# Kernel optimization log

Hardware: AMD Instinct MI355X
Metric: run time of the kernel (lower is better)

## Reference

```python
import jax, jax.numpy as jnp
import numpy as np

HIDDEN = 1024
NUM_HEADS = 8
HEAD_DIM = HIDDEN // NUM_HEADS
MAX_BACKWARD = 11   # context_left - 1
MAX_FORWARD = 12    # context_right
SPAN = MAX_BACKWARD + MAX_FORWARD + 1  # 24

B, U, W, C = 8, 16, 128, 151


def setup_inputs() -> dict:
    key = jax.random.key(0)
    kq, kk, kp = jax.random.split(key, 3)
    queries = jax.random.normal(kq, (B, U, W, NUM_HEADS, HEAD_DIM), dtype=jnp.float32)
    keys = jax.random.normal(kk, (B, U, C, NUM_HEADS, HEAD_DIM), dtype=jnp.float32)
    # glorot-ish scale for pos_proj (hidden, num_heads*head_dim)
    pos_proj = jax.random.normal(kp, (HIDDEN, NUM_HEADS * HEAD_DIM), dtype=jnp.float32) * (1.0 / np.sqrt(HIDDEN))
    return {"queries": queries, "keys": keys, "pos_proj": pos_proj}


def _sinusoid_emb(pos_proj):
    # positions: max_backward .. -max_forward (descending), shape (SPAN,)
    pos = jnp.arange(MAX_BACKWARD, -(MAX_FORWARD + 1), -1, dtype=jnp.float32)
    num_ts = HIDDEN // 2
    inv_ts = jnp.ones((num_ts,), dtype=jnp.float32)  # module uses ones
    scaled = pos[:, None] * inv_ts[None, :]          # (SPAN, HIDDEN/2)
    signal = jnp.concatenate([jnp.sin(scaled), jnp.cos(scaled)], axis=-1)  # (SPAN, HIDDEN)
    proj = signal @ pos_proj                         # (SPAN, N*H)
    return proj.reshape(SPAN, NUM_HEADS, HEAD_DIM)


def _relative_shift(term_bd, context_size):
    # term_bd: (B, N, U, W, SPAN) -> (B, N, U, W, C)
    b, n, u, w, _ = term_bd.shape
    pad = context_size + 1 - SPAN
    padded = jnp.pad(term_bd, ((0, 0), (0, 0), (0, 0), (0, 0), (0, pad)))
    flat = padded.reshape(b, n, u, w * (context_size + 1))
    sliced = flat[:, :, :, : w * context_size]
    return sliced.reshape(b, n, u, w, context_size)


def reference(queries, keys, pos_proj):
    context_size = keys.shape[2]
    sin_emb = _sinusoid_emb(pos_proj)                      # (SPAN, N, H)
    qp = jnp.transpose(queries, (0, 3, 1, 2, 4))           # (B, N, U, W, H)
    kp = jnp.transpose(keys, (0, 3, 1, 4, 2))              # (B, N, U, H, C)
    term_ac = jnp.matmul(qp, kp)                           # (B, N, U, W, C)
    # term_bd: query-position interaction, (B, N, U, W, SPAN)
    term_bd = jnp.einsum("bnuwh,fnh->bnuwf", qp, sin_emb)
    term_bd = _relative_shift(term_bd, context_size)       # (B, N, U, W, C)
    return term_ac + term_bd
```

## Files before the change

kernel.cpp:

```cpp
#include <hip/hip_runtime.h>
#include <cmath>

#define NHEADS 8
#define HDIM 128
#define SPAN 24
#define U_ 16
#define W_ 128
#define C_ 151
#define HID 1024

typedef unsigned short ushort8v __attribute__((ext_vector_type(8)));
typedef __bf16 bf16x8 __attribute__((ext_vector_type(8)));
typedef float f32x4 __attribute__((ext_vector_type(4)));

__device__ inline unsigned short f2bf(float f) {
    union { float f; unsigned u; } v; v.f = f;
    unsigned r = v.u + 0x7FFFu + ((v.u >> 16) & 1u);
    return (unsigned short)(r >> 16);
}
__device__ inline float bf2f(unsigned short u) {
    union { unsigned u; float f; } v; v.u = ((unsigned)u) << 16;
    return v.f;
}

__global__ void k_partial(const float* __restrict__ pp, float* __restrict__ part) {
    const int t = threadIdx.x;
    const int row0 = blockIdx.x * 16;
    float4 s = make_float4(0.f, 0.f, 0.f, 0.f);
    #pragma unroll
    for (int i = 0; i < 16; ++i) {
        float4 v = *(const float4*)(pp + (size_t)(row0 + i) * HID + t * 4);
        s.x += v.x; s.y += v.y; s.z += v.z; s.w += v.w;
    }
    *(float4*)(part + (size_t)blockIdx.x * HID + t * 4) = s;
}

struct SC { float s[SPAN]; float c[SPAN]; };

__global__ void k_emb(const float* __restrict__ part, unsigned short* __restrict__ emb, SC sc) {
    const int j = blockIdx.x * 256 + threadIdx.x;
    float s1 = 0.f, s2 = 0.f;
    #pragma unroll 4
    for (int i = 0; i < 32; ++i) s1 += part[(size_t)i * HID + j];
    #pragma unroll 4
    for (int i = 32; i < 64; ++i) s2 += part[(size_t)i * HID + j];
    #pragma unroll
    for (int f = 0; f < SPAN; ++f)
        emb[(size_t)f * HID + j] = f2bf(sc.s[f] * s1 + sc.c[f] * s2);
}

#define KEXT_BYTES (176 * 256)
#define BD_PITCH 25

__global__ __launch_bounds__(512, 6) void k_main(const float* __restrict__ q,
                                                 const float* __restrict__ k,
                                                 const unsigned short* __restrict__ emb,
                                                 float* __restrict__ out) {
    __shared__ __align__(16) char lds_raw[KEXT_BYTES + W_ * BD_PITCH * 2];
    unsigned short* bd = (unsigned short*)(lds_raw + KEXT_BYTES);

    const int bid = (blockIdx.x & 7) * 128 + (blockIdx.x >> 3);
    const int n = bid & 7;
    const int u = (bid >> 3) & 15;
    const int b = bid >> 7;

    const size_t qbase = ((size_t)(b * U_ + u) * W_) * HID + n * HDIM;
    const size_t kbase = ((size_t)(b * U_ + u) * C_) * HID + n * HDIM;
    const size_t obase = ((size_t)((b * NHEADS + n) * U_ + u)) * (W_ * C_);

    const int tid = threadIdx.x;
    const int lane = tid & 63;
    const int wave = tid >> 6;
    const int w0 = wave * 16;
    const int lr = lane & 15;
    const int lk = lane >> 4;

    for (int ui = tid; ui < 176 * 16; ui += 512) {
        const int r = ui >> 4, u16 = ui & 15;
        const int dst = r * 256 + ((u16 * 16) ^ ((r & 7) << 4));
        ushort8v val;
        if (r < C_) {
            const float* src = k + kbase + (size_t)r * HID + u16 * 8;
            float4 f0 = *(const float4*)src;
            float4 f1 = *(const float4*)(src + 4);
            val[0] = f2bf(f0.x); val[1] = f2bf(f0.y); val[2] = f2bf(f0.z); val[3] = f2bf(f0.w);
            val[4] = f2bf(f1.x); val[5] = f2bf(f1.y); val[6] = f2bf(f1.z); val[7] = f2bf(f1.w);
        } else if (r < 175) {
            val = *(const ushort8v*)(emb + (size_t)(r - C_) * HID + n * HDIM + u16 * 8);
        } else {
            val = (ushort8v)(unsigned short)0;
        }
        *(ushort8v*)(lds_raw + dst) = val;
    }

    const float* qrow = q + qbase + (size_t)(w0 + lr) * HID + lk * 8;
    float4 qa[8];
    #pragma unroll
    for (int kk = 0; kk < 4; ++kk) {
        qa[2 * kk]     = *(const float4*)(qrow + kk * 32);
        qa[2 * kk + 1] = *(const float4*)(qrow + kk * 32 + 4);
    }
    bf16x8 qf[4];
    #pragma unroll
    for (int kk = 0; kk < 4; ++kk) {
        float4 a0 = qa[2 * kk];
        float4 a1 = qa[2 * kk + 1];
        ushort8v au;
        au[0] = f2bf(a0.x); au[1] = f2bf(a0.y); au[2] = f2bf(a0.z); au[3] = f2bf(a0.w);
        au[4] = f2bf(a1.x); au[5] = f2bf(a1.y); au[6] = f2bf(a1.z); au[7] = f2bf(a1.w);
        qf[kk] = __builtin_bit_cast(bf16x8, au);
    }
    __syncthreads();

    f32x4 acc[11];
    #pragma unroll
    for (int j = 0; j < 11; ++j) acc[j] = (f32x4)(0.f);

    #pragma unroll
    for (int kk = 0; kk < 4; ++kk) {
        #pragma unroll
        for (int j = 0; j < 11; ++j) {
            const int r = j * 16 + lr;
            const int byt = r * 256 + (((kk * 64) + (lk * 16)) ^ ((r & 7) << 4));
            bf16x8 bf = __builtin_bit_cast(bf16x8, *(const ushort8v*)(lds_raw + byt));
            acc[j] = __builtin_amdgcn_mfma_f32_16x16x32_bf16(qf[kk], bf, acc[j], 0, 0, 0);
        }
    }

    {
        const int c9 = 144 + lr;
        if (c9 >= C_) {
            const int f = c9 - C_;
            #pragma unroll
            for (int reg = 0; reg < 4; ++reg) {
                const int w = w0 + lk * 4 + reg;
                bd[w * BD_PITCH + f] = f2bf(acc[9][reg]);
            }
        }
        const int f10 = 9 + lr;
        if (f10 < SPAN) {
            #pragma unroll
            for (int reg = 0; reg < 4; ++reg) {
                const int w = w0 + lk * 4 + reg;
                bd[w * BD_PITCH + f10] = f2bf(acc[10][reg]);
            }
        }
    }

    #pragma unroll
    for (int j = 0; j < 10; ++j) {
        const int c = j * 16 + lr;
        if (c < C_) {
            #pragma unroll
            for (int reg = 0; reg < 4; ++reg) {
                const int w = w0 + lk * 4 + reg;
                float v = acc[j][reg];
                const int d = c - w;
                if (d >= 0 && d < SPAN) v += bf2f(bd[w * BD_PITCH + d]);
                out[obase + (size_t)w * C_ + c] = v;
            }
        }
    }
}

extern "C" void kernel_launch(void* const* d_in, const int* in_sizes, int n_in,
                              void* d_out, int out_size, void* d_ws, size_t ws_size,
                              hipStream_t stream) {
    const float* queries = (const float*)d_in[0];
    const float* keys    = (const float*)d_in[1];
    const float* posproj = (const float*)d_in[2];
    float* out = (float*)d_out;

    float* part = (float*)d_ws;
    unsigned short* emb = (unsigned short*)((char*)d_ws + 64 * HID * 4);

    SC sc;
    for (int f = 0; f < SPAN; ++f) {
        float p = (float)(11 - f);
        sc.s[f] = sinf(p);
        sc.c[f] = cosf(p);
    }

    k_partial<<<64, 256, 0, stream>>>(posproj, part);
    k_emb<<<4, 256, 0, stream>>>(part, emb, sc);
    k_main<<<1024, 512, 0, stream>>>(queries, keys, emb, out);
}
```

Before: 59.23 us.

## Make main kernel process four tiles per block with double-buffered LDS prefetch

Result: faster. 57.94 us (-2.2%).

```diff
diff --git a/kernel.cpp b/kernel.cpp
--- a/kernel.cpp
+++ b/kernel.cpp
@@ -21,6 +21,12 @@
 __device__ inline float bf2f(unsigned short u) {
     union { unsigned u; float f; } v; v.u = ((unsigned)u) << 16;
     return v.f;
+}
+__device__ inline ushort8v cvt8(float4 a, float4 b) {
+    ushort8v v;
+    v[0] = f2bf(a.x); v[1] = f2bf(a.y); v[2] = f2bf(a.z); v[3] = f2bf(a.w);
+    v[4] = f2bf(b.x); v[5] = f2bf(b.y); v[6] = f2bf(b.z); v[7] = f2bf(b.w);
+    return v;
 }
 
 __global__ void k_partial(const float* __restrict__ pp, float* __restrict__ part) {
@@ -37,7 +43,7 @@
 
 struct SC { float s[SPAN]; float c[SPAN]; };
 
-__global__ void k_emb(const float* __restrict__ part, unsigned short* __restrict__ emb, SC sc) {
+__global__ void k_emb(const float* __restrict__ part, float* __restrict__ emb, SC sc) {
     const int j = blockIdx.x * 256 + threadIdx.x;
     float s1 = 0.f, s2 = 0.f;
     #pragma unroll 4
@@ -46,27 +52,79 @@
     for (int i = 32; i < 64; ++i) s2 += part[(size_t)i * HID + j];
     #pragma unroll
     for (int f = 0; f < SPAN; ++f)
-        emb[(size_t)f * HID + j] = f2bf(sc.s[f] * s1 + sc.c[f] * s2);
-}
-
-#define KEXT_BYTES (176 * 256)
+        emb[(size_t)f * HID + j] = sc.s[f] * s1 + sc.c[f] * s2;
+}
+
+#define KB 45056
 #define BD_PITCH 25
-
-__global__ __launch_bounds__(512, 6) void k_main(const float* __restrict__ q,
+#define NITER 4
+
+
+#define STAGE_LOAD(TILE)                                                        \
+    {                                                                           \
+        const int n_ = (TILE) & 7;                                              \
+        const int u_ = ((TILE) >> 3) & 15;                                      \
+        const int b_ = (TILE) >> 7;                                             \
+        const size_t kb_ = ((size_t)(b_ * U_ + u_) * C_) * HID + n_ * HDIM;     \
+        _Pragma("unroll")                                                       \
+        for (int it = 0; it < 4; ++it) {                                        \
+            const int ui = it * 512 + tid;                                      \
+            const int r = ui >> 4, u16 = ui & 15;                               \
+            const float* src = k + kb_ + (size_t)r * HID + u16 * 8;             \
+            pf0[it] = *(const float4*)src;                                      \
+            pf1[it] = *(const float4*)(src + 4);                                \
+        }                                                                       \
+        {                                                                       \
+            const int ui = 4 * 512 + tid;                                       \
+            const int r = ui >> 4, u16 = ui & 15;                               \
+            const float* src = (r < C_)                                         \
+                ? (k + kb_ + (size_t)r * HID + u16 * 8)                         \
+                : (embf + (size_t)(r - C_) * HID + n_ * HDIM + u16 * 8);        \
+            pf0[4] = *(const float4*)src;                                       \
+            pf1[4] = *(const float4*)(src + 4);                                 \
+        }                                                                       \
+        if (tid < 256) {                                                        \
+            const int r = 160 + (tid >> 4), u16 = tid & 15;                     \
+            if (r < 175) {                                                      \
+                const float* src = embf + (size_t)(r - C_) * HID + n_ * HDIM + u16 * 8; \
+                pt0 = *(const float4*)src;                                      \
+                pt1 = *(const float4*)(src + 4);                                \
+            }                                                                   \
+        }                                                                       \
+        const size_t qb_ = ((size_t)(b_ * U_ + u_) * W_) * HID + n_ * HDIM;     \
+        const float* qrow_ = q + qb_ + (size_t)(w0 + lr) * HID + lk * 8;        \
+        _Pragma("unroll")                                                       \
+        for (int kk = 0; kk < 4; ++kk) {                                        \
+            qpf[2 * kk]     = *(const float4*)(qrow_ + kk * 32);                \
+            qpf[2 * kk + 1] = *(const float4*)(qrow_ + kk * 32 + 4);            \
+        }                                                                       \
+    }
+
+#define STAGE_WRITE(BUF)                                                        \
+    {                                                                           \
+        _Pragma("unroll")                                                       \
+        for (int it = 0; it < 5; ++it) {                                        \
+            const int ui = it * 512 + tid;                                      \
+            const int r = ui >> 4, u16 = ui & 15;                               \
+            const int dst = r * 256 + ((u16 * 16) ^ ((r & 7) << 4));            \
+            *(ushort8v*)((BUF) + dst) = cvt8(pf0[it], pf1[it]);                 \
+        }                                                                       \
+        if (tid < 256) {                                                        \
+            const int r = 160 + (tid >> 4), u16 = tid & 15;                     \
+            const int dst = r * 256 + ((u16 * 16) ^ ((r & 7) << 4));            \
+            ushort8v v_;                                                        \
+            if (r < 175) v_ = cvt8(pt0, pt1);                                   \
+            else         v_ = (ushort8v)(unsigned short)0;                      \
+            *(ushort8v*)((BUF) + dst) = v_;                                     \
+        }                                                                       \
+    }
+
+__global__ __launch_bounds__(512, 2) void k_main(const float* __restrict__ q,
                                                  const float* __restrict__ k,
-                                                 const unsigned short* __restrict__ emb,
+                                                 const float* __restrict__ embf,
                                                  float* __restrict__ out) {
-    __shared__ __align__(16) char lds_raw[KEXT_BYTES + W_ * BD_PITCH * 2];
-    unsigned short* bd = (unsigned short*)(lds_raw + KEXT_BYTES);
-
-    const int bid = (blockIdx.x & 7) * 128 + (blockIdx.x >> 3);
-    const int n = bid & 7;
-    const int u = (bid >> 3) & 15;
-    const int b = bid >> 7;
-
-    const size_t qbase = ((size_t)(b * U_ + u) * W_) * HID + n * HDIM;
-    const size_t kbase = ((size_t)(b * U_ + u) * C_) * HID + n * HDIM;
-    const size_t obase = ((size_t)((b * NHEADS + n) * U_ + u)) * (W_ * C_);
+    __shared__ __align__(16) char lds_raw[2 * KB + W_ * BD_PITCH * 2];
+    unsigned short* bd = (unsigned short*)(lds_raw + 2 * KB);
 
     const int tid = threadIdx.x;
     const int lane = tid & 63;
@@ -75,91 +133,86 @@
     const int lr = lane & 15;
     const int lk = lane >> 4;
 
-    for (int ui = tid; ui < 176 * 16; ui += 512) {
-        const int r = ui >> 4, u16 = ui & 15;
-        const int dst = r * 256 + ((u16 * 16) ^ ((r & 7) << 4));
-        ushort8v val;
-        if (r < C_) {
-            const float* src = k + kbase + (size_t)r * HID + u16 * 8;
-            float4 f0 = *(const float4*)src;
-            float4 f1 = *(const float4*)(src + 4);
-            val[0] = f2bf(f0.x); val[1] = f2bf(f0.y); val[2] = f2bf(f0.z); val[3] = f2bf(f0.w);
-            val[4] = f2bf(f1.x); val[5] = f2bf(f1.y); val[6] = f2bf(f1.z); val[7] = f2bf(f1.w);
-        } else if (r < 175) {
-            val = *(const ushort8v*)(emb + (size_t)(r - C_) * HID + n * HDIM + u16 * 8);
-        } else {
-            val = (ushort8v)(unsigned short)0;
+    const int logical = (blockIdx.x & 7) * 32 + (blockIdx.x >> 3);
+    const int tile0 = logical * NITER;
+
+    float4 pf0[5], pf1[5], pt0, pt1, qpf[8];
+
+    STAGE_LOAD(tile0);
+    STAGE_WRITE(lds_raw);
+    __syncthreads();
+
+    for (int i = 0; i < NITER; ++i) {
+        const int tile = tile0 + i;
+        char* bufc = lds_raw + (i & 1) * KB;
+        char* bufn = lds_raw + ((i & 1) ^ 1) * KB;
+
+        bf16x8 qf[4];
+        #pragma unroll
+        for (int kk = 0; kk < 4; ++kk)
+            qf[kk] = __builtin_bit_cast(bf16x8, cvt8(qpf[2 * kk], qpf[2 * kk + 1]));
+
+        if (i + 1 < NITER) STAGE_LOAD(tile + 1);
+
+        f32x4 acc[11];
+        #pragma unroll
+        for (int j = 0; j < 11; ++j) acc[j] = (f32x4)(0.f);
+
+        #pragma unroll
+        for (int kk = 0; kk < 4; ++kk) {
+            #pragma unroll
+            for (int j = 0; j < 11; ++j) {
+                const int r = j * 16 + lr;
+                const int byt = r * 256 + (((kk * 64) + (lk * 16)) ^ ((r & 7) << 4));
+                bf16x8 bf = __builtin_bit_cast(bf16x8, *(const ushort8v*)(bufc + byt));
+                acc[j] = __builtin_amdgcn_mfma_f32_16x16x32_bf16(qf[kk], bf, acc[j], 0, 0, 0);
+            }
         }
-        *(ushort8v*)(lds_raw + dst) = val;
-    }
-
-    const float* qrow = q + qbase + (size_t)(w0 + lr) * HID + lk * 8;
-    float4 qa[8];
-    #pragma unroll
-    for (int kk = 0; kk < 4; ++kk) {
-        qa[2 * kk]     = *(const float4*)(qrow + kk * 32);
-        qa[2 * kk + 1] = *(const float4*)(qrow + kk * 32 + 4);
-    }
-    bf16x8 qf[4];
-    #pragma unroll
-    for (int kk = 0; kk < 4; ++kk) {
-        float4 a0 = qa[2 * kk];
-        float4 a1 = qa[2 * kk + 1];
-        ushort8v au;
-        au[0] = f2bf(a0.x); au[1] = f2bf(a0.y); au[2] = f2bf(a0.z); au[3] = f2bf(a0.w);
-        au[4] = f2bf(a1.x); au[5] = f2bf(a1.y); au[6] = f2bf(a1.z); au[7] = f2bf(a1.w);
-        qf[kk] = __builtin_bit_cast(bf16x8, au);
-    }
-    __syncthreads();
-
-    f32x4 acc[11];
-    #pragma unroll
-    for (int j = 0; j < 11; ++j) acc[j] = (f32x4)(0.f);
-
-    #pragma unroll
-    for (int kk = 0; kk < 4; ++kk) {
-        #pragma unroll
-        for (int j = 0; j < 11; ++j) {
-            const int r = j * 16 + lr;
-            const int byt = r * 256 + (((kk * 64) + (lk * 16)) ^ ((r & 7) << 4));
-            bf16x8 bf = __builtin_bit_cast(bf16x8, *(const ushort8v*)(lds_raw + byt));
-            acc[j] = __builtin_amdgcn_mfma_f32_16x16x32_bf16(qf[kk], bf, acc[j], 0, 0, 0);
+
+        if (i + 1 < NITER) STAGE_WRITE(bufn);
+
+        {
+            const int c9 = 144 + lr;
+            if (c9 >= C_) {
+                const int f = c9 - C_;
+                #pragma unroll
+                for (int reg = 0; reg < 4; ++reg) {
+                    const int w = w0 + lk * 4 + reg;
+                    bd[w * BD_PITCH + f] = f2bf(acc[9][reg]);
+                }
+            }
+            const int f10 = 9 + lr;
+            if (f10 < SPAN) {
+                #pragma unroll
+                for (int reg = 0; reg < 4; ++reg) {
+                    const int w = w0 + lk * 4 + reg;
+                    bd[w * BD_PITCH + f10] = f2bf(acc[10][reg]);
+                }
+            }
         }
-    }
-
-    {
-        const int c9 = 144 + lr;
-        if (c9 >= C_) {
-            const int f = c9 - C_;
+
+        {
+            const int n_ = tile & 7;
+            const int u_ = (tile >> 3) & 15;
+            const int b_ = tile >> 7;
+            const size_t ob_ = ((size_t)((b_ * NHEADS + n_) * U_ + u_)) * (W_ * C_);
             #pragma unroll
-            for (int reg = 0; reg < 4; ++reg) {
-                const int w = w0 + lk * 4 + reg;
-                bd[w * BD_PITCH + f] = f2bf(acc[9][reg]);
+            for (int j = 0; j < 10; ++j) {
+                const int c = j * 16 + lr;
+                if (c < C_) {
+                    #pragma unroll
+                    for (int reg = 0; reg < 4; ++reg) {
+                        const int w = w0 + lk * 4 + reg;
+                        float v = acc[j][reg];
+                        const int d = c - w;
+                        if (d >= 0 && d < SPAN) v += bf2f(bd[w * BD_PITCH + d]);
+                        out[ob_ + (size_t)w * C_ + c] = v;
+                    }
+                }
             }
         }
-        const int f10 = 9 + lr;
-        if (f10 < SPAN) {
-            #pragma unroll
-            for (int reg = 0; reg < 4; ++reg) {
-                const int w = w0 + lk * 4 + reg;
-                bd[w * BD_PITCH + f10] = f2bf(acc[10][reg]);
-            }
-        }
-    }
-
-    #pragma unroll
-    for (int j = 0; j < 10; ++j) {
-        const int c = j * 16 + lr;
-        if (c < C_) {
-            #pragma unroll
-            for (int reg = 0; reg < 4; ++reg) {
-                const int w = w0 + lk * 4 + reg;
-                float v = acc[j][reg];
-                const int d = c - w;
-                if (d >= 0 && d < SPAN) v += bf2f(bd[w * BD_PITCH + d]);
-                out[obase + (size_t)w * C_ + c] = v;
-            }
-        }
+
+        __syncthreads();
     }
 }
 
@@ -172,7 +225,7 @@
     float* out = (float*)d_out;
 
     float* part = (float*)d_ws;
-    unsigned short* emb = (unsigned short*)((char*)d_ws + 64 * HID * 4);
+    float* embf = (float*)((char*)d_ws + 64 * HID * 4);
 
     SC sc;
     for (int f = 0; f < SPAN; ++f) {
@@ -182,6 +235,6 @@
     }
 
     k_partial<<<64, 256, 0, stream>>>(posproj, part);
-    k_emb<<<4, 256, 0, stream>>>(part, emb, sc);
-    k_main<<<1024, 512, 0, stream>>>(queries, keys, emb, out);
-}
+    k_emb<<<4, 256, 0, stream>>>(part, embf, sc);
+    k_main<<<256, 512, 0, stream>>>(queries, keys, embf, out);
+}
```

## Batch all global loads before LDS conversion stores in main kernel

Applied to the files above, without the earlier changes.

After: 57.45 us. 3.0% less time.

```diff
diff --git a/kernel.cpp b/kernel.cpp
--- a/kernel.cpp
+++ b/kernel.cpp
@@ -22,6 +22,12 @@
     union { unsigned u; float f; } v; v.u = ((unsigned)u) << 16;
     return v.f;
 }
+__device__ inline ushort8v cvt8(float4 a, float4 b) {
+    ushort8v v;
+    v[0] = f2bf(a.x); v[1] = f2bf(a.y); v[2] = f2bf(a.z); v[3] = f2bf(a.w);
+    v[4] = f2bf(b.x); v[5] = f2bf(b.y); v[6] = f2bf(b.z); v[7] = f2bf(b.w);
+    return v;
+}
 
 __global__ void k_partial(const float* __restrict__ pp, float* __restrict__ part) {
     const int t = threadIdx.x;
@@ -37,7 +43,7 @@
 
 struct SC { float s[SPAN]; float c[SPAN]; };
 
-__global__ void k_emb(const float* __restrict__ part, unsigned short* __restrict__ emb, SC sc) {
+__global__ void k_emb(const float* __restrict__ part, float* __restrict__ emb, SC sc) {
     const int j = blockIdx.x * 256 + threadIdx.x;
     float s1 = 0.f, s2 = 0.f;
     #pragma unroll 4
@@ -46,20 +52,20 @@
     for (int i = 32; i < 64; ++i) s2 += part[(size_t)i * HID + j];
     #pragma unroll
     for (int f = 0; f < SPAN; ++f)
-        emb[(size_t)f * HID + j] = f2bf(sc.s[f] * s1 + sc.c[f] * s2);
+        emb[(size_t)f * HID + j] = sc.s[f] * s1 + sc.c[f] * s2;
 }
 
 #define KEXT_BYTES (176 * 256)
 #define BD_PITCH 25
 
-__global__ __launch_bounds__(512, 6) void k_main(const float* __restrict__ q,
+__global__ __launch_bounds__(512, 4) void k_main(const float* __restrict__ q,
                                                  const float* __restrict__ k,
-                                                 const unsigned short* __restrict__ emb,
+                                                 const float* __restrict__ embf,
                                                  float* __restrict__ out) {
     __shared__ __align__(16) char lds_raw[KEXT_BYTES + W_ * BD_PITCH * 2];
     unsigned short* bd = (unsigned short*)(lds_raw + KEXT_BYTES);
 
-    const int bid = (blockIdx.x & 7) * 128 + (blockIdx.x >> 3);
+    const int bid = blockIdx.x;
     const int n = bid & 7;
     const int u = (bid >> 3) & 15;
     const int b = bid >> 7;
@@ -75,41 +81,54 @@
     const int lr = lane & 15;
     const int lk = lane >> 4;
 
-    for (int ui = tid; ui < 176 * 16; ui += 512) {
+    float4 pf0[5], pf1[5], pt0, pt1;
+    #pragma unroll
+    for (int it = 0; it < 5; ++it) {
+        const int ui = it * 512 + tid;
+        const int r = ui >> 4, u16 = ui & 15;
+        const float* src = (r < C_)
+            ? (k + kbase + (size_t)r * HID + u16 * 8)
+            : (embf + (size_t)(r - C_) * HID + n * HDIM + u16 * 8);
+        pf0[it] = *(const float4*)src;
+        pf1[it] = *(const float4*)(src + 4);
+    }
+    if (tid < 256) {
+        const int r = 160 + (tid >> 4), u16 = tid & 15;
+        if (r < 175) {
+            const float* src = embf + (size_t)(r - C_) * HID + n * HDIM + u16 * 8;
+            pt0 = *(const float4*)src;
+            pt1 = *(const float4*)(src + 4);
+        }
+    }
+    const float* qrow = q + qbase + (size_t)(w0 + lr) * HID + lk * 8;
+    float4 qpf[8];
+    #pragma unroll
+    for (int kk = 0; kk < 4; ++kk) {
+        qpf[2 * kk]     = *(const float4*)(qrow + kk * 32);
+        qpf[2 * kk + 1] = *(const float4*)(qrow + kk * 32 + 4);
+    }
+
+    #pragma unroll
+    for (int it = 0; it < 5; ++it) {
+        const int ui = it * 512 + tid;
         const int r = ui >> 4, u16 = ui & 15;
         const int dst = r * 256 + ((u16 * 16) ^ ((r & 7) << 4));
-        ushort8v val;
-        if (r < C_) {
-            const float* src = k + kbase + (size_t)r * HID + u16 * 8;
-            float4 f0 = *(const float4*)src;
-            float4 f1 = *(const float4*)(src + 4);
-            val[0] = f2bf(f0.x); val[1] = f2bf(f0.y); val[2] = f2bf(f0.z); val[3] = f2bf(f0.w);
-            val[4] = f2bf(f1.x); val[5] = f2bf(f1.y); val[6] = f2bf(f1.z); val[7] = f2bf(f1.w);
-        } else if (r < 175) {
-            val = *(const ushort8v*)(emb + (size_t)(r - C_) * HID + n * HDIM + u16 * 8);
-        } else {
-            val = (ushort8v)(unsigned short)0;
-        }
-        *(ushort8v*)(lds_raw + dst) = val;
-    }
-
-    const float* qrow = q + qbase + (size_t)(w0 + lr) * HID + lk * 8;
-    float4 qa[8];
-    #pragma unroll
-    for (int kk = 0; kk < 4; ++kk) {
-        qa[2 * kk]     = *(const float4*)(qrow + kk * 32);
-        qa[2 * kk + 1] = *(const float4*)(qrow + kk * 32 + 4);
-    }
+        *(ushort8v*)(lds_raw + dst) = cvt8(pf0[it], pf1[it]);
+    }
+    if (tid < 256) {
+        const int r = 160 + (tid >> 4), u16 = tid & 15;
+        const int dst = r * 256 + ((u16 * 16) ^ ((r & 7) << 4));
+        ushort8v v_;
+        if (r < 175) v_ = cvt8(pt0, pt1);
+        else         v_ = (ushort8v)(unsigned short)0;
+        *(ushort8v*)(lds_raw + dst) = v_;
+    }
+
     bf16x8 qf[4];
     #pragma unroll
-    for (int kk = 0; kk < 4; ++kk) {
-        float4 a0 = qa[2 * kk];
-        float4 a1 = qa[2 * kk + 1];
-        ushort8v au;
-        au[0] = f2bf(a0.x); au[1] = f2bf(a0.y); au[2] = f2bf(a0.z); au[3] = f2bf(a0.w);
-        au[4] = f2bf(a1.x); au[5] = f2bf(a1.y); au[6] = f2bf(a1.z); au[7] = f2bf(a1.w);
-        qf[kk] = __builtin_bit_cast(bf16x8, au);
-    }
+    for (int kk = 0; kk < 4; ++kk)
+        qf[kk] = __builtin_bit_cast(bf16x8, cvt8(qpf[2 * kk], qpf[2 * kk + 1]));
+
     __syncthreads();
 
     f32x4 acc[11];
@@ -172,7 +191,7 @@
     float* out = (float*)d_out;
 
     float* part = (float*)d_ws;
-    unsigned short* emb = (unsigned short*)((char*)d_ws + 64 * HID * 4);
+    float* embf = (float*)((char*)d_ws + 64 * HID * 4);
 
     SC sc;
     for (int f = 0; f < SPAN; ++f) {
@@ -182,6 +201,6 @@
     }
 
     k_partial<<<64, 256, 0, stream>>>(posproj, part);
-    k_emb<<<4, 256, 0, stream>>>(part, emb, sc);
-    k_main<<<1024, 512, 0, stream>>>(queries, keys, emb, out);
-}
+    k_emb<<<4, 256, 0, stream>>>(part, embf, sc);
+    k_main<<<1024, 512, 0, stream>>>(queries, keys, embf, out);
+}
```
